# Kernel tuning notes

Hardware: AMD Instinct MI355X
Metric: run time of the kernel (lower is better)

Reference implementation:

```python
import jax, jax.numpy as jnp
import numpy as np
from jax import lax

B, CIN, COUT, H, W = 16, 128, 128, 128, 128
KH, KW = 3, 3
BLK_O, BLK_I = 32, 32          # block sizes over (out_ch, in_ch); kernel dims fully covered
PRUNING_RATE = 0.75


def _make_block_mask():
    # Reproduces blocksparse(): keep (1 - pruning_rate) of the channel blocks.
    nbo, nbi = COUT // BLK_O, CIN // BLK_I
    n_blocks = nbo * nbi
    n_keep = int(round(n_blocks * (1.0 - PRUNING_RATE)))
    rng = np.random.default_rng(42)
    keep = np.zeros(n_blocks, dtype=np.float32)
    keep[rng.permutation(n_blocks)[:n_keep]] = 1.0
    blk = keep.reshape(nbo, nbi)                     # [4, 4]
    m = np.kron(blk, np.ones((BLK_O, BLK_I), np.float32))   # [COUT, CIN]
    m = np.broadcast_to(m[:, :, None, None], (COUT, CIN, KH, KW))
    return jnp.asarray(np.ascontiguousarray(m))


def setup_inputs() -> dict:
    key = jax.random.key(0)
    k1, k2, k3 = jax.random.split(key, 3)
    x = jax.random.normal(k1, (B, CIN, H, W), dtype=jnp.float32)
    weight = jax.random.normal(k2, (COUT, CIN, KH, KW), dtype=jnp.float32) * 0.05
    bias = jax.random.normal(k3, (COUT,), dtype=jnp.float32) * 0.05
    mask = _make_block_mask()
    return {"x": x, "weight": weight, "bias": bias, "mask": mask}


def reference(x, weight, bias, mask):
    # weight = weight * mask, then standard dense conv2d (stride 1, pad 1, dil 1, groups 1)
    w = weight * mask
    y = lax.conv_general_dilated(
        x, w,
        window_strides=(1, 1),
        padding=((1, 1), (1, 1)),
        dimension_numbers=("NCHW", "OIHW", "NCHW"),
    )
    return y + bias[None, :, None, None]
```

## Files before the change

kernel.cpp:

```cpp
#include <hip/hip_runtime.h>

#define NBATCH 16
#define CIN_ 128
#define COUT_ 128
#define H_ 128
#define W_ 128
#define TH 4
#define NR (TH + 2)
#define CPITCH 34

typedef short bf16x8 __attribute__((ext_vector_type(8)));
typedef float f32x4 __attribute__((ext_vector_type(4)));

__device__ __forceinline__ unsigned short f32_to_bf16(float f) {
  unsigned int u = __float_as_uint(f);
  u += 0x7fffu + ((u >> 16) & 1u);
  return (unsigned short)(u >> 16);
}

__global__ void make_lists_k(const float* __restrict__ mask, int* __restrict__ lists) {
  if (threadIdx.x == 0) {
    for (int i = 0; i < 20; ++i) lists[i] = 0;
    for (int ob = 0; ob < 4; ++ob) {
      int c = 0;
      for (int ib = 0; ib < 4; ++ib) {
        float v = mask[(size_t)((ob * 32) * CIN_ + ib * 32) * 9];
        if (v != 0.0f) { lists[4 + ob * 4 + c] = ib; ++c; }
      }
      lists[ob] = c;
    }
  }
}

__global__ __launch_bounds__(256) void pack_w_k(const float* __restrict__ weight,
                                                const float* __restrict__ mask,
                                                const int* __restrict__ lists,
                                                unsigned short* __restrict__ wpack) {
  const int khkw = blockIdx.x;
  const int slot = blockIdx.y;
  const int ob   = blockIdx.z;
  if (slot >= lists[ob]) return;
  const int ib = lists[4 + ob * 4 + slot];
  const int kh = khkw / 3, kw = khkw % 3;
  for (int e = threadIdx.x; e < 1024; e += 256) {
    const int co = e >> 5, ci = e & 31;
    const int cog = ob * 32 + co, cig = ib * 32 + ci;
    const size_t widx = ((size_t)(cog * CIN_ + cig) * 3 + kh) * 3 + kw;
    const float v = weight[widx] * mask[widx];
    wpack[(size_t)((ob * 4 + slot) * 9 + khkw) * 1024 + e] = f32_to_bf16(v);
  }
}

__global__ __launch_bounds__(256, 3) void conv_fused_k(const float* __restrict__ x,
                                                       const unsigned short* __restrict__ wpack,
                                                       const int* __restrict__ lists,
                                                       const float* __restrict__ bias,
                                                       float* __restrict__ out) {
  __shared__ unsigned short xs[NR * 130 * CPITCH];

  const int tid  = threadIdx.x;
  const int wave = tid >> 6;
  const int lane = tid & 63;
  const int wl   = lane & 15;
  const int kg   = lane >> 4;

  const int h0 = blockIdx.x * TH;
  const int b  = blockIdx.y;
  const int ob = blockIdx.z;
  const int w0 = wave * 32;

  const int cnt = lists[ob];

  f32x4 acc[TH][2][2] = {};

  const int q = tid & 31;
  const int g = tid >> 5;

  for (int s = 0; s < cnt; ++s) {
    const int ib = lists[4 + ob * 4 + s];

    if (s) __syncthreads();

    {
      const float* xbase = x + ((size_t)b * CIN_ + ib * 32) * H_ * W_ + q * 4;
#pragma unroll
      for (int it = 0; it < 12; ++it) {
        const int combo = it * 8 + g;
        const int r  = combo >> 4;
        const int cp = combo & 15;
        const int row = h0 - 1 + r;
        const bool rv = (row >= 0) && (row < H_);
        const float* src = xbase + ((size_t)(cp * 2) * H_ + (rv ? row : 0)) * W_;
        f32x4 va = *(const f32x4*)src;
        f32x4 vb = *(const f32x4*)(src + (size_t)H_ * W_);
        unsigned int* xd = (unsigned int*)(xs + (r * 130 + q * 4 + 1) * CPITCH + cp * 2);
#pragma unroll
        for (int j = 0; j < 4; ++j) {
          unsigned int lo = rv ? (unsigned int)f32_to_bf16(va[j]) : 0u;
          unsigned int hi = rv ? (unsigned int)f32_to_bf16(vb[j]) : 0u;
          xd[j * (CPITCH / 2)] = lo | (hi << 16);
        }
      }
      for (int e = tid; e < NR * 2 * 32; e += 256) {
        const int r = e >> 6, edge = (e >> 5) & 1, ci = e & 31;
        xs[(r * 130 + (edge ? 129 : 0)) * CPITCH + ci] = 0;
      }
    }

    const unsigned short* wk =
        wpack + (size_t)((ob * 4 + s) * 9) * 1024 + wl * 32 + kg * 8;
    bf16x8 a[3][3][2];
#pragma unroll
    for (int kh = 0; kh < 3; ++kh)
#pragma unroll
      for (int kw = 0; kw < 3; ++kw) {
        a[kh][kw][0] = *(const bf16x8*)(wk + (kh * 3 + kw) * 1024);
        a[kh][kw][1] = *(const bf16x8*)(wk + (kh * 3 + kw) * 1024 + 16 * 32);
      }

    __syncthreads();

#pragma unroll
    for (int ridx = 0; ridx < NR; ++ridx) {
      bf16x8 bf[2][3];
#pragma unroll
      for (int ni = 0; ni < 2; ++ni)
#pragma unroll
        for (int kw = 0; kw < 3; ++kw)
          bf[ni][kw] = *(const bf16x8*)(xs + (ridx * 130 + w0 + ni * 16 + wl + kw) * CPITCH + kg * 8);

#pragma unroll
      for (int kh = 0; kh < 3; ++kh) {
        const int hi = ridx - kh;
        if (hi < 0 || hi >= TH) continue;
#pragma unroll
        for (int kw = 0; kw < 3; ++kw) {
          acc[hi][0][0] = __builtin_amdgcn_mfma_f32_16x16x32_bf16(a[kh][kw][0], bf[0][kw], acc[hi][0][0], 0, 0, 0);
          acc[hi][0][1] = __builtin_amdgcn_mfma_f32_16x16x32_bf16(a[kh][kw][0], bf[1][kw], acc[hi][0][1], 0, 0, 0);
          acc[hi][1][0] = __builtin_amdgcn_mfma_f32_16x16x32_bf16(a[kh][kw][1], bf[0][kw], acc[hi][1][0], 0, 0, 0);
          acc[hi][1][1] = __builtin_amdgcn_mfma_f32_16x16x32_bf16(a[kh][kw][1], bf[1][kw], acc[hi][1][1], 0, 0, 0);
        }
      }
    }
  }

#pragma unroll
  for (int mi = 0; mi < 2; ++mi)
#pragma unroll
    for (int j = 0; j < 4; ++j) {
      const int co = mi * 16 + kg * 4 + j;
      const float bv = bias[ob * 32 + co];
#pragma unroll
      for (int hh = 0; hh < TH; ++hh) {
        float* yrow = out + ((size_t)(b * COUT_ + ob * 32 + co) * H_ + h0 + hh) * W_;
        yrow[w0 + wl]      = acc[hh][mi][0][j] + bv;
        yrow[w0 + wl + 16] = acc[hh][mi][1][j] + bv;
      }
    }
}

extern "C" void kernel_launch(void* const* d_in, const int* in_sizes, int n_in,
                              void* d_out, int out_size, void* d_ws, size_t ws_size,
                              hipStream_t stream) {
  const float* x      = (const float*)d_in[0];
  const float* weight = (const float*)d_in[1];
  const float* bias   = (const float*)d_in[2];
  const float* mask   = (const float*)d_in[3];
  float* out = (float*)d_out;

  int* lists = (int*)d_ws;
  unsigned short* wpack = (unsigned short*)((char*)d_ws + 4096);

  make_lists_k<<<1, 64, 0, stream>>>(mask, lists);
  pack_w_k<<<dim3(9, 4, 4), 256, 0, stream>>>(weight, mask, lists, wpack);
  conv_fused_k<<<dim3(H_ / TH, NBATCH, 4), 256, 0, stream>>>(x, wpack, lists, bias, out);
}
```

Baseline: 74.49 us.

## Warp-specialize conv into producer/consumer waves with double-buffered LDS tiles

The conv kernel becomes a persistent-style kernel with 512 threads. Four producer waves load and convert the next input tile into one of two LDS buffers while four consumer waves run the MFMAs on the current buffer. Each of the 256 workgroups loops over 8 (batch, out-block) units for a fixed row tile, which overlaps global loads with compute. In exchange it doubles LDS use, halves the number of waves doing MFMA work, and serializes the work into fewer blocks with a barrier every step.

Result: slower. 79.63 us (+6.9%).

```diff
diff --git a/kernel.cpp b/kernel.cpp
--- a/kernel.cpp
+++ b/kernel.cpp
@@ -8,6 +8,7 @@
 #define TH 4
 #define NR (TH + 2)
 #define CPITCH 34
+#define TILE_ELEMS (NR * 130 * CPITCH)
 
 typedef short bf16x8 __attribute__((ext_vector_type(8)));
 typedef float f32x4 __attribute__((ext_vector_type(4)));
@@ -51,37 +52,49 @@
   }
 }
 
-__global__ __launch_bounds__(256, 3) void conv_fused_k(const float* __restrict__ x,
-                                                       const unsigned short* __restrict__ wpack,
-                                                       const int* __restrict__ lists,
-                                                       const float* __restrict__ bias,
-                                                       float* __restrict__ out) {
-  __shared__ unsigned short xs[NR * 130 * CPITCH];
-
-  const int tid  = threadIdx.x;
+__global__ __launch_bounds__(512, 2) void conv_pc_k(const float* __restrict__ x,
+                                                    const unsigned short* __restrict__ wpack,
+                                                    const int* __restrict__ lists,
+                                                    const float* __restrict__ bias,
+                                                    float* __restrict__ out) {
+  __shared__ unsigned short xs[2][TILE_ELEMS];
+
+  const int tid = threadIdx.x;
+  const int wg  = blockIdx.x;
+  const bool is_prod = tid >= 256;
+
+  int cnts[4];
+#pragma unroll
+  for (int o = 0; o < 4; ++o) cnts[o] = lists[o];
+
+  int U = 0;
+#pragma unroll
+  for (int i = 0; i < 8; ++i) { int c = cnts[i & 3]; U += (c > 0 ? c : 1); }
+
+  const int h0 = (wg >> 3) * TH;
+
+  const int ptid = tid & 255;
+  const int q = ptid & 31;
+  const int g = ptid >> 5;
+
+  const int lane = tid & 63;
   const int wave = tid >> 6;
-  const int lane = tid & 63;
   const int wl   = lane & 15;
   const int kg   = lane >> 4;
-
-  const int h0 = blockIdx.x * TH;
-  const int b  = blockIdx.y;
-  const int ob = blockIdx.z;
-  const int w0 = wave * 32;
-
-  const int cnt = lists[ob];
+  const int w0   = (wave & 3) * 32;
 
   f32x4 acc[TH][2][2] = {};
 
-  const int q = tid & 31;
-  const int g = tid >> 5;
-
-  for (int s = 0; s < cnt; ++s) {
-    const int ib = lists[4 + ob * 4 + s];
-
-    if (s) __syncthreads();
-
-    {
+  int pi = 0, ps = 0;
+  int ci_ = 0, cs = 0;
+
+  if (is_prod) {
+    const int ob = pi & 3;
+    const int c  = cnts[ob];
+    if (c > 0) {
+      const int b  = (wg * 2 + (pi >> 2)) & 15;
+      const int ib = lists[4 + ob * 4 + ps];
+      unsigned short* buf = xs[0];
       const float* xbase = x + ((size_t)b * CIN_ + ib * 32) * H_ * W_ + q * 4;
 #pragma unroll
       for (int it = 0; it < 12; ++it) {
@@ -93,7 +106,7 @@
         const float* src = xbase + ((size_t)(cp * 2) * H_ + (rv ? row : 0)) * W_;
         f32x4 va = *(const f32x4*)src;
         f32x4 vb = *(const f32x4*)(src + (size_t)H_ * W_);
-        unsigned int* xd = (unsigned int*)(xs + (r * 130 + q * 4 + 1) * CPITCH + cp * 2);
+        unsigned int* xd = (unsigned int*)(buf + (r * 130 + q * 4 + 1) * CPITCH + cp * 2);
 #pragma unroll
         for (int j = 0; j < 4; ++j) {
           unsigned int lo = rv ? (unsigned int)f32_to_bf16(va[j]) : 0u;
@@ -101,62 +114,125 @@
           xd[j * (CPITCH / 2)] = lo | (hi << 16);
         }
       }
-      for (int e = tid; e < NR * 2 * 32; e += 256) {
-        const int r = e >> 6, edge = (e >> 5) & 1, ci = e & 31;
-        xs[(r * 130 + (edge ? 129 : 0)) * CPITCH + ci] = 0;
+      for (int e = ptid; e < NR * 2 * 32; e += 256) {
+        const int r = e >> 6, edge = (e >> 5) & 1, cc = e & 31;
+        buf[(r * 130 + (edge ? 129 : 0)) * CPITCH + cc] = 0;
       }
     }
-
-    const unsigned short* wk =
-        wpack + (size_t)((ob * 4 + s) * 9) * 1024 + wl * 32 + kg * 8;
-    bf16x8 a[3][3][2];
-#pragma unroll
-    for (int kh = 0; kh < 3; ++kh)
-#pragma unroll
-      for (int kw = 0; kw < 3; ++kw) {
-        a[kh][kw][0] = *(const bf16x8*)(wk + (kh * 3 + kw) * 1024);
-        a[kh][kw][1] = *(const bf16x8*)(wk + (kh * 3 + kw) * 1024 + 16 * 32);
-      }
-
+  }
+  __syncthreads();
+
+  for (int k = 0; k < U; ++k) {
+    if (is_prod) {
+      {
+        const int ob = pi & 3;
+        const int nu = (cnts[ob] > 0 ? cnts[ob] : 1);
+        if (ps + 1 < nu) ++ps; else { ++pi; ps = 0; }
+      }
+      if (k + 1 < U) {
+        const int ob = pi & 3;
+        const int c  = cnts[ob];
+        if (c > 0) {
+          const int b  = (wg * 2 + (pi >> 2)) & 15;
+          const int ib = lists[4 + ob * 4 + ps];
+          unsigned short* buf = xs[(k + 1) & 1];
+          const float* xbase = x + ((size_t)b * CIN_ + ib * 32) * H_ * W_ + q * 4;
+#pragma unroll
+          for (int it = 0; it < 12; ++it) {
+            const int combo = it * 8 + g;
+            const int r  = combo >> 4;
+            const int cp = combo & 15;
+            const int row = h0 - 1 + r;
+            const bool rv = (row >= 0) && (row < H_);
+            const float* src = xbase + ((size_t)(cp * 2) * H_ + (rv ? row : 0)) * W_;
+            f32x4 va = *(const f32x4*)src;
+            f32x4 vb = *(const f32x4*)(src + (size_t)H_ * W_);
+            unsigned int* xd = (unsigned int*)(buf + (r * 130 + q * 4 + 1) * CPITCH + cp * 2);
+#pragma unroll
+            for (int j = 0; j < 4; ++j) {
+              unsigned int lo = rv ? (unsigned int)f32_to_bf16(va[j]) : 0u;
+              unsigned int hi = rv ? (unsigned int)f32_to_bf16(vb[j]) : 0u;
+              xd[j * (CPITCH / 2)] = lo | (hi << 16);
+            }
+          }
+          for (int e = ptid; e < NR * 2 * 32; e += 256) {
+            const int r = e >> 6, edge = (e >> 5) & 1, cc = e & 31;
+            buf[(r * 130 + (edge ? 129 : 0)) * CPITCH + cc] = 0;
+          }
+        }
+      }
+    } else {
+      const int ob  = ci_ & 3;
+      const int cnt = cnts[ob];
+      const int b   = (wg * 2 + (ci_ >> 2)) & 15;
+
+      if (cnt > 0) {
+        const int s = cs;
+        const unsigned short* xsb = xs[k & 1];
+
+        const unsigned short* wk =
+            wpack + (size_t)((ob * 4 + s) * 9) * 1024 + wl * 32 + kg * 8;
+        bf16x8 a[3][3][2];
+#pragma unroll
+        for (int kh = 0; kh < 3; ++kh)
+#pragma unroll
+          for (int kw = 0; kw < 3; ++kw) {
+            a[kh][kw][0] = *(const bf16x8*)(wk + (kh * 3 + kw) * 1024);
+            a[kh][kw][1] = *(const bf16x8*)(wk + (kh * 3 + kw) * 1024 + 16 * 32);
+          }
+
+#pragma unroll
+        for (int ridx = 0; ridx < NR; ++ridx) {
+          bf16x8 bf[2][3];
+#pragma unroll
+          for (int ni = 0; ni < 2; ++ni)
+#pragma unroll
+            for (int kw = 0; kw < 3; ++kw)
+              bf[ni][kw] = *(const bf16x8*)(xsb + (ridx * 130 + w0 + ni * 16 + wl + kw) * CPITCH + kg * 8);
+
+#pragma unroll
+          for (int kh = 0; kh < 3; ++kh) {
+            const int hi = ridx - kh;
+            if (hi < 0 || hi >= TH) continue;
+#pragma unroll
+            for (int kw = 0; kw < 3; ++kw) {
+              acc[hi][0][0] = __builtin_amdgcn_mfma_f32_16x16x32_bf16(a[kh][kw][0], bf[0][kw], acc[hi][0][0], 0, 0, 0);
+              acc[hi][0][1] = __builtin_amdgcn_mfma_f32_16x16x32_bf16(a[kh][kw][0], bf[1][kw], acc[hi][0][1], 0, 0, 0);
+              acc[hi][1][0] = __builtin_amdgcn_mfma_f32_16x16x32_bf16(a[kh][kw][1], bf[0][kw], acc[hi][1][0], 0, 0, 0);
+              acc[hi][1][1] = __builtin_amdgcn_mfma_f32_16x16x32_bf16(a[kh][kw][1], bf[1][kw], acc[hi][1][1], 0, 0, 0);
+            }
+          }
+        }
+      }
+
+      const int nu = (cnt > 0 ? cnt : 1);
+      if (cs == nu - 1) {
+#pragma unroll
+        for (int mi = 0; mi < 2; ++mi)
+#pragma unroll
+          for (int j = 0; j < 4; ++j) {
+            const int co = mi * 16 + kg * 4 + j;
+            const float bv = bias[ob * 32 + co];
+#pragma unroll
+            for (int hh = 0; hh < TH; ++hh) {
+              float* yrow = out + ((size_t)(b * COUT_ + ob * 32 + co) * H_ + h0 + hh) * W_;
+              yrow[w0 + wl]      = acc[hh][mi][0][j] + bv;
+              yrow[w0 + wl + 16] = acc[hh][mi][1][j] + bv;
+            }
+          }
+#pragma unroll
+        for (int hh = 0; hh < TH; ++hh)
+#pragma unroll
+          for (int mi = 0; mi < 2; ++mi)
+#pragma unroll
+            for (int ni = 0; ni < 2; ++ni)
+              acc[hh][mi][ni] = f32x4{0.f, 0.f, 0.f, 0.f};
+      }
+
+      if (cs + 1 < nu) ++cs; else { ++ci_; cs = 0; }
+    }
     __syncthreads();
-
-#pragma unroll
-    for (int ridx = 0; ridx < NR; ++ridx) {
-      bf16x8 bf[2][3];
-#pragma unroll
-      for (int ni = 0; ni < 2; ++ni)
-#pragma unroll
-        for (int kw = 0; kw < 3; ++kw)
-          bf[ni][kw] = *(const bf16x8*)(xs + (ridx * 130 + w0 + ni * 16 + wl + kw) * CPITCH + kg * 8);
-
-#pragma unroll
-      for (int kh = 0; kh < 3; ++kh) {
-        const int hi = ridx - kh;
-        if (hi < 0 || hi >= TH) continue;
-#pragma unroll
-        for (int kw = 0; kw < 3; ++kw) {
-          acc[hi][0][0] = __builtin_amdgcn_mfma_f32_16x16x32_bf16(a[kh][kw][0], bf[0][kw], acc[hi][0][0], 0, 0, 0);
-          acc[hi][0][1] = __builtin_amdgcn_mfma_f32_16x16x32_bf16(a[kh][kw][0], bf[1][kw], acc[hi][0][1], 0, 0, 0);
-          acc[hi][1][0] = __builtin_amdgcn_mfma_f32_16x16x32_bf16(a[kh][kw][1], bf[0][kw], acc[hi][1][0], 0, 0, 0);
-          acc[hi][1][1] = __builtin_amdgcn_mfma_f32_16x16x32_bf16(a[kh][kw][1], bf[1][kw], acc[hi][1][1], 0, 0, 0);
-        }
-      }
-    }
-  }
-
-#pragma unroll
-  for (int mi = 0; mi < 2; ++mi)
-#pragma unroll
-    for (int j = 0; j < 4; ++j) {
-      const int co = mi * 16 + kg * 4 + j;
-      const float bv = bias[ob * 32 + co];
-#pragma unroll
-      for (int hh = 0; hh < TH; ++hh) {
-        float* yrow = out + ((size_t)(b * COUT_ + ob * 32 + co) * H_ + h0 + hh) * W_;
-        yrow[w0 + wl]      = acc[hh][mi][0][j] + bv;
-        yrow[w0 + wl + 16] = acc[hh][mi][1][j] + bv;
-      }
-    }
+  }
 }
 
 extern "C" void kernel_launch(void* const* d_in, const int* in_sizes, int n_in,
@@ -173,5 +249,5 @@
 
   make_lists_k<<<1, 64, 0, stream>>>(mask, lists);
   pack_w_k<<<dim3(9, 4, 4), 256, 0, stream>>>(weight, mask, lists, wpack);
-  conv_fused_k<<<dim3(H_ / TH, NBATCH, 4), 256, 0, stream>>>(x, wpack, lists, bias, out);
-}
+  conv_pc_k<<<256, 512, 0, stream>>>(x, wpack, lists, bias, out);
+}
```
